# Optimization experiments

Measured on AMD Instinct MI355X. Metric: run time of the kernel, lower is better.

Reference implementation:

```python
import jax, jax.numpy as jnp
import numpy as np

N_NODES = 20000   # max_childs
N_EDGES = 640000
FEAT = 256        # node_feat_size
HID = 128         # node_hidden_size
NUM_SEM = 57
EDGE_TYPES = 4
EDGE_FEAT = 8


def setup_inputs() -> dict:
    key = jax.random.key(0)
    ks = jax.random.split(key, 10)
    inp = {
        "child_feats": jax.random.normal(ks[0], (1, N_NODES, FEAT + NUM_SEM), jnp.float32),
        "child_exists": jnp.ones((1, N_NODES, 1), jnp.float32),
        "edge_type_onehot": jax.random.uniform(ks[1], (1, N_EDGES, EDGE_TYPES), jnp.float32),
        "edge_feats": jax.random.normal(ks[2], (1, N_EDGES, EDGE_FEAT), jnp.float32),
        "edge_indices": jax.random.randint(ks[3], (1, N_EDGES, 2), 0, N_NODES, jnp.int64 if jax.config.jax_enable_x64 else jnp.int32),
        "W_child": jax.random.normal(ks[4], (FEAT + NUM_SEM, HID), jnp.float32) * 0.05,
        "b_child": jnp.zeros((HID,), jnp.float32),
        "W_edge0": jax.random.normal(ks[5], (2 * HID + EDGE_FEAT + EDGE_TYPES, HID), jnp.float32) * 0.05,
        "b_edge0": jnp.zeros((HID,), jnp.float32),
        "W_edge1": jax.random.normal(ks[6], (2 * HID + EDGE_FEAT + EDGE_TYPES, HID), jnp.float32) * 0.05,
        "b_edge1": jnp.zeros((HID,), jnp.float32),
        "W_parent": jax.random.normal(ks[7], (3 * HID, FEAT), jnp.float32) * 0.05,
        "b_parent": jnp.zeros((FEAT,), jnp.float32),
    }
    return inp


def reference(child_feats, child_exists, edge_type_onehot, edge_feats, edge_indices,
              W_child, b_child, W_edge0, b_edge0, W_edge1, b_edge1, W_parent, b_parent):
    # child_op + existence mask: [1, N, FEAT+NUM_SEM] -> [N, HID]
    h = jax.nn.relu(child_feats @ W_child + b_child) * child_exists
    h = h[0]  # batch_size is hard-coded to 1 in the original module

    # symmetric_type == 'max': pool over children
    iter_parent_feats = [jnp.max(h, axis=0)]

    # edge features: cat(edge_type_onehot, edge_feats) -> [E, ET+EF]
    ef = jnp.concatenate([edge_type_onehot[0], edge_feats[0]], axis=1)
    src = edge_indices[0, :, 0]
    dst = edge_indices[0, :, 1]

    for W, b in ((W_edge0, b_edge0), (W_edge1, b_edge1)):
        # gather -> per-edge MLP: [E, 2*HID + ET + EF] -> [E, HID]
        msg = jax.nn.relu(jnp.concatenate([h[src], h[dst], ef], axis=1) @ W + b)
        # edge_symmetric_type == 'max' with zero-initialized out buffer:
        # result = max(0, segment_max(msg)) per node
        h = jnp.maximum(jax.ops.segment_max(msg, src, num_segments=N_NODES), 0.0)
        iter_parent_feats.append(jnp.max(h, axis=0))

    parent = jnp.concatenate(iter_parent_feats)[None, :]  # [1, 3*HID]
    return jax.nn.relu(parent @ W_parent + b_parent)       # [1, FEAT]
```

## Files before the change

### kernel.cpp

```cpp
#include <hip/hip_runtime.h>

#define N_NODES   20000
#define N_EDGES   640000
#define CF        313
#define KC        320
#define ROWB      640

typedef __attribute__((ext_vector_type(8))) short short8;
typedef __attribute__((ext_vector_type(4))) float f32x4;
typedef __attribute__((ext_vector_type(4))) unsigned short u16x4;
typedef _Float16 h2 __attribute__((ext_vector_type(2)));

static __device__ __forceinline__ unsigned short f2bf(float f) {
    unsigned u = __float_as_uint(f);
    u = u + 0x7FFFu + ((u >> 16) & 1u);
    return (unsigned short)(u >> 16);
}
static __device__ __forceinline__ int pkh(float a, float b) {
    h2 h; h.x = (_Float16)a; h.y = (_Float16)b;
    return __builtin_bit_cast(int, h);
}
static __device__ __forceinline__ h2 bch(int v) { return __builtin_bit_cast(h2, v); }
static __device__ __forceinline__ float dot2f(h2 a, h2 b, float c) {
    return __builtin_amdgcn_fdot2(a, b, c, false);
}

__global__ void setup_kernel(const float* __restrict__ Wc,
                             const float* __restrict__ We0,
                             const float* __restrict__ We1,
                             const int* __restrict__ eidx,
                             const float* __restrict__ cf,
                             unsigned short* __restrict__ WcT,
                             unsigned short* __restrict__ Wab0,
                             unsigned short* __restrict__ Wab1,
                             unsigned* __restrict__ hist,
                             unsigned short* __restrict__ cfp) {
    const int b = blockIdx.x, tid = threadIdx.x;
    if (b < 416) {
        int g = b * 256 + tid;
        if (g < 128 * KC) {
            int n = g / KC, k = g % KC;
            WcT[g] = f2bf(k < CF ? Wc[k * 128 + n] : 0.f);
        } else if (g < 128 * KC + 32768) {
            int h = g - 128 * KC;
            int n = h >> 7, k = h & 127;
            Wab0[h] = f2bf(n < 128 ? We0[k * 128 + n] : We0[(128 + k) * 128 + (n - 128)]);
        } else {
            int h = g - 128 * KC - 32768;
            int n = h >> 7, k = h & 127;
            Wab1[h] = f2bf(n < 128 ? We1[k * 128 + n] : We1[(128 + k) * 128 + (n - 128)]);
        }
    } else if (b < 2916) {
        int e = (b - 416) * 256 + tid;
        if (e < N_EDGES) atomicAdd(hist + eidx[2 * e], 1u);
    } else {
        int g = (b - 2916) * 256 + tid;
        if (g < 800000) {
            int node = g / 40, c = g - node * 40;
            const float* base = cf + (size_t)node * CF;
            short8 v = {};
            #pragma unroll
            for (int kk = 0; kk < 8; ++kk) {
                int k = c * 8 + kk;
                if (k < CF) v[kk] = (short)f2bf(base[k]);
            }
            *(short8*)(cfp + (size_t)g * 8) = v;
        }
    }
}

__global__ void scan_kernel(const unsigned* __restrict__ hist,
                            unsigned* __restrict__ cursor,
                            unsigned* __restrict__ cstart) {
    __shared__ unsigned part[1024];
    int t = threadIdx.x;
    unsigned loc[20];
    unsigned s = 0;
    int base = t * 20;
    if (t < 1000) {
        #pragma unroll
        for (int i = 0; i < 20; ++i) { loc[i] = hist[base + i]; s += loc[i]; }
    }
    part[t] = s;
    __syncthreads();
    for (int off = 1; off < 1024; off <<= 1) {
        unsigned u = (t >= off) ? part[t - off] : 0u;
        __syncthreads();
        part[t] += u;
        __syncthreads();
    }
    if (t < 1000) {
        unsigned run = part[t] - s;
        #pragma unroll
        for (int i = 0; i < 20; ++i) {
            cursor[base + i] = run;
            cstart[base + i] = run;
            run += loc[i];
        }
    }
}

__global__ void scatter_kernel(const int* __restrict__ eidx,
                               const float* __restrict__ onehot,
                               const float* __restrict__ efeat,
                               unsigned* __restrict__ cursor,
                               int4* __restrict__ es) {
    int e = blockIdx.x * 256 + threadIdx.x;
    if (e >= N_EDGES) return;
    int2 sd = ((const int2*)eidx)[e];
    unsigned pos = atomicAdd(cursor + sd.x, 1u);
    float4 oh = *(const float4*)(onehot + 4 * (size_t)e);
    float4 ea = *(const float4*)(efeat + 8 * (size_t)e);
    float4 eb = *(const float4*)(efeat + 8 * (size_t)e + 4);
    int4 w0, w1;
    w0.x = sd.y;
    w0.y = pkh(oh.x, oh.y); w0.z = pkh(oh.z, oh.w); w0.w = pkh(ea.x, ea.y);
    w1.x = pkh(ea.z, ea.w); w1.y = pkh(eb.x, eb.y); w1.z = pkh(eb.z, eb.w); w1.w = 0;
    es[2 * (size_t)pos]     = w0;
    es[2 * (size_t)pos + 1] = w1;
}

__global__ __launch_bounds__(256, 2)
void child_gemm(const unsigned short* __restrict__ cfp,
                const float* __restrict__ exists,
                const unsigned short* __restrict__ WT,
                const float* __restrict__ bias,
                unsigned short* __restrict__ hbf,
                unsigned int* __restrict__ pmax) {
    __shared__ __align__(16) unsigned char Alds[64 * ROWB];

    const int tid  = threadIdx.x;
    const int lane = tid & 63;
    const int wave = tid >> 6;
    const int n0   = wave * 32;
    const int row0 = blockIdx.x * 64;

    short8 bfrag[10][2];
    {
        int col  = n0 + (lane & 15);
        int krow = (lane >> 4) * 8;
        #pragma unroll
        for (int ks = 0; ks < 10; ++ks)
            #pragma unroll
            for (int nt = 0; nt < 2; ++nt)
                bfrag[ks][nt] = *(const short8*)(WT + (col + nt * 16) * KC + ks * 32 + krow);
    }
    float bv[2];
    bv[0] = bias[n0 + (lane & 15)];
    bv[1] = bias[n0 + 16 + (lane & 15)];

    {
        int r = tid >> 2, p = tid & 3;
        int node = row0 + r;
        bool valid = node < N_NODES;
        unsigned rbase = r * ROWB;
        unsigned sw = (r & 7) << 4;
        #pragma unroll
        for (int i = 0; i < 10; ++i) {
            int c = p + i * 4;
            short8 v = {};
            if (valid) v = *(const short8*)(cfp + (size_t)node * KC + c * 8);
            *(short8*)(Alds + ((rbase + c * 16) ^ sw)) = v;
        }
    }
    __syncthreads();

    f32x4 acc[4][2] = {};
    {
        int arow = lane & 15;
        unsigned kb = (lane >> 4) * 16;
        #pragma unroll
        for (int ks = 0; ks < 10; ++ks)
            #pragma unroll
            for (int mt = 0; mt < 4; ++mt) {
                int row = mt * 16 + arow;
                short8 a = *(const short8*)(Alds + (((unsigned)row * ROWB + ks * 64 + kb) ^ ((row & 7) << 4)));
                acc[mt][0] = __builtin_amdgcn_mfma_f32_16x16x32_bf16(a, bfrag[ks][0], acc[mt][0], 0, 0, 0);
                acc[mt][1] = __builtin_amdgcn_mfma_f32_16x16x32_bf16(a, bfrag[ks][1], acc[mt][1], 0, 0, 0);
            }
    }

    {
        int rb = (lane >> 4) * 4;
        #pragma unroll
        for (int nt = 0; nt < 2; ++nt) {
            int col = n0 + nt * 16 + (lane & 15);
            float m = 0.f;
            #pragma unroll
            for (int mt = 0; mt < 4; ++mt)
                #pragma unroll
                for (int j = 0; j < 4; ++j) {
                    int node = row0 + mt * 16 + rb + j;
                    float v = 0.f;
                    if (node < N_NODES) {
                        v = fmaxf(acc[mt][nt][j] + bv[nt], 0.f) * exists[node];
                        hbf[node * 128 + col] = f2bf(v);
                    }
                    m = fmaxf(m, v);
                }
            m = fmaxf(m, __shfl_xor(m, 16));
            m = fmaxf(m, __shfl_xor(m, 32));
            if ((lane >> 4) == 0)
                atomicMax(pmax + col, __float_as_uint(m));
        }
    }
}

__global__ __launch_bounds__(256)
void gemmAB(const unsigned short* __restrict__ hbf,
            const unsigned short* __restrict__ WT,
            const float* __restrict__ bias,
            float* __restrict__ Afl,
            unsigned short* __restrict__ Bbf) {
    const int tid  = threadIdx.x;
    const int lane = tid & 63;
    const int wave = tid >> 6;
    const int n0   = wave * 64;
    const int row0 = blockIdx.x * 64;
    const int krow = (lane >> 4) * 8;

    short8 bfrag[4][4];
    {
        int colb = n0 + (lane & 15);
        #pragma unroll
        for (int ks = 0; ks < 4; ++ks)
            #pragma unroll
            for (int nt = 0; nt < 4; ++nt)
                bfrag[ks][nt] = *(const short8*)(WT + (colb + nt * 16) * 128 + ks * 32 + krow);
    }

    f32x4 acc[4][4] = {};
    #pragma unroll
    for (int ks = 0; ks < 4; ++ks)
        #pragma unroll
        for (int mt = 0; mt < 4; ++mt) {
            int row = row0 + mt * 16 + (lane & 15);
            row = min(row, N_NODES - 1);
            short8 a = *(const short8*)(hbf + (size_t)row * 128 + ks * 32 + krow);
            #pragma unroll
            for (int nt = 0; nt < 4; ++nt)
                acc[mt][nt] = __builtin_amdgcn_mfma_f32_16x16x32_bf16(a, bfrag[ks][nt], acc[mt][nt], 0, 0, 0);
        }

    {
        int rb = (lane >> 4) * 4;
        #pragma unroll
        for (int nt = 0; nt < 4; ++nt) {
            int col = n0 + nt * 16 + (lane & 15);
            float badd = (col < 128) ? bias[col] : 0.f;
            #pragma unroll
            for (int mt = 0; mt < 4; ++mt)
                #pragma unroll
                for (int j = 0; j < 4; ++j) {
                    int row = row0 + mt * 16 + rb + j;
                    if (row < N_NODES) {
                        float v = acc[mt][nt][j] + badd;
                        if (col < 128) Afl[(size_t)row * 128 + col] = v;
                        else           Bbf[(size_t)row * 128 + col - 128] = f2bf(v);
                    }
                }
        }
    }
}

__global__ __launch_bounds__(256)
void edge_pass(const unsigned short* __restrict__ Bbf,
               const float* __restrict__ Afl,
               const int4* __restrict__ es,
               const float* __restrict__ Wef,
               const unsigned* __restrict__ cstart,
               const unsigned* __restrict__ hist,
               unsigned short* __restrict__ hbf,
               unsigned* __restrict__ pslice) {
    __shared__ unsigned cmax[128];
    const int tid = threadIdx.x;
    if (tid < 128) cmax[tid] = 0;
    __syncthreads();

    const int s  = blockIdx.x * 8 + (tid >> 5);
    const int c0 = (tid & 31) * 4;

    h2 wf[6][4];
    #pragma unroll
    for (int kp = 0; kp < 6; ++kp)
        #pragma unroll
        for (int j = 0; j < 4; ++j) {
            h2 w;
            w.x = (_Float16)Wef[(2 * kp) * 128 + c0 + j];
            w.y = (_Float16)Wef[(2 * kp + 1) * 128 + c0 + j];
            wf[kp][j] = w;
        }

    float m0 = -1e30f, m1 = -1e30f, m2 = -1e30f, m3 = -1e30f;
    const unsigned cnt = hist[s];
    if (cnt) {
        const int4* p = es + 2 * (size_t)cstart[s];
        const unsigned last = cnt - 1;
        unsigned j1 = min(1u, last), j2 = min(2u, last), j3 = min(3u, last);
        int4 ra0 = p[0],      rb0 = p[1];
        int4 ra1 = p[2 * j1], rb1 = p[2 * j1 + 1];
        int4 ra2 = p[2 * j2], rb2 = p[2 * j2 + 1];
        int4 ra3 = p[2 * j3], rb3 = p[2 * j3 + 1];
        u16x4 b0 = *(const u16x4*)(Bbf + (size_t)(unsigned)ra0.x * 128 + c0);
        u16x4 b1 = *(const u16x4*)(Bbf + (size_t)(unsigned)ra1.x * 128 + c0);
        u16x4 b2 = *(const u16x4*)(Bbf + (size_t)(unsigned)ra2.x * 128 + c0);
        #pragma unroll 4
        for (unsigned i = 0; i < cnt; ++i) {
            u16x4 b3 = *(const u16x4*)(Bbf + (size_t)(unsigned)ra3.x * 128 + c0);
            unsigned j4 = min(i + 4, last);
            int4 ra4 = p[2 * j4], rb4 = p[2 * j4 + 1];

            h2 e0 = bch(ra0.y), e1 = bch(ra0.z), e2 = bch(ra0.w);
            h2 e3 = bch(rb0.x), e4 = bch(rb0.y), e5 = bch(rb0.z);

            float x0 = __uint_as_float(((unsigned)(unsigned short)b0[0]) << 16);
            float x1 = __uint_as_float(((unsigned)(unsigned short)b0[1]) << 16);
            float x2 = __uint_as_float(((unsigned)(unsigned short)b0[2]) << 16);
            float x3 = __uint_as_float(((unsigned)(unsigned short)b0[3]) << 16);
            x0 = dot2f(e0, wf[0][0], x0); x1 = dot2f(e0, wf[0][1], x1);
            x2 = dot2f(e0, wf[0][2], x2); x3 = dot2f(e0, wf[0][3], x3);
            x0 = dot2f(e1, wf[1][0], x0); x1 = dot2f(e1, wf[1][1], x1);
            x2 = dot2f(e1, wf[1][2], x2); x3 = dot2f(e1, wf[1][3], x3);
            x0 = dot2f(e2, wf[2][0], x0); x1 = dot2f(e2, wf[2][1], x1);
            x2 = dot2f(e2, wf[2][2], x2); x3 = dot2f(e2, wf[2][3], x3);
            x0 = dot2f(e3, wf[3][0], x0); x1 = dot2f(e3, wf[3][1], x1);
            x2 = dot2f(e3, wf[3][2], x2); x3 = dot2f(e3, wf[3][3], x3);
            x0 = dot2f(e4, wf[4][0], x0); x1 = dot2f(e4, wf[4][1], x1);
            x2 = dot2f(e4, wf[4][2], x2); x3 = dot2f(e4, wf[4][3], x3);
            x0 = dot2f(e5, wf[5][0], x0); x1 = dot2f(e5, wf[5][1], x1);
            x2 = dot2f(e5, wf[5][2], x2); x3 = dot2f(e5, wf[5][3], x3);
            m0 = fmaxf(m0, x0); m1 = fmaxf(m1, x1);
            m2 = fmaxf(m2, x2); m3 = fmaxf(m3, x3);

            ra0 = ra1; rb0 = rb1; ra1 = ra2; rb1 = rb2;
            ra2 = ra3; rb2 = rb3; ra3 = ra4; rb3 = rb4;
            b0 = b1; b1 = b2; b2 = b3;
        }
    }

    float4 a = *(const float4*)(Afl + (size_t)s * 128 + c0);
    float h0 = fmaxf(a.x + m0, 0.f), h1 = fmaxf(a.y + m1, 0.f);
    float h2v = fmaxf(a.z + m2, 0.f), h3 = fmaxf(a.w + m3, 0.f);

    unsigned lo = (unsigned)f2bf(h0) | ((unsigned)f2bf(h1) << 16);
    unsigned hi = (unsigned)f2bf(h2v) | ((unsigned)f2bf(h3) << 16);
    *(uint2*)(hbf + (size_t)s * 128 + c0) = make_uint2(lo, hi);

    float g0 = fmaxf(h0, __shfl_xor(h0, 32));
    float g1 = fmaxf(h1, __shfl_xor(h1, 32));
    float g2 = fmaxf(h2v, __shfl_xor(h2v, 32));
    float g3 = fmaxf(h3, __shfl_xor(h3, 32));
    if ((tid & 63) < 32) {
        atomicMax(&cmax[c0],     __float_as_uint(g0));
        atomicMax(&cmax[c0 + 1], __float_as_uint(g1));
        atomicMax(&cmax[c0 + 2], __float_as_uint(g2));
        atomicMax(&cmax[c0 + 3], __float_as_uint(g3));
    }
    __syncthreads();
    if (tid < 128) atomicMax(pslice + tid, cmax[tid]);
}

__global__ void final_gemm(const float* __restrict__ parent,
                           const float* __restrict__ Wp,
                           const float* __restrict__ bp,
                           float* __restrict__ out) {
    __shared__ float p[384];
    __shared__ float red[1024];
    int t = threadIdx.x;
    if (t < 384) p[t] = parent[t];
    __syncthreads();
    int col = t & 255, kc = t >> 8;
    float s = 0.f;
    for (int k = kc * 96; k < kc * 96 + 96; ++k) s += p[k] * Wp[k * 256 + col];
    red[t] = s;
    __syncthreads();
    if (kc == 0)
        out[col] = fmaxf(red[col] + red[col + 256] + red[col + 512] + red[col + 768] + bp[col], 0.f);
}

extern "C" void kernel_launch(void* const* d_in, const int* in_sizes, int n_in,
                              void* d_out, int out_size, void* d_ws, size_t ws_size,
                              hipStream_t stream) {
    const float* child_feats  = (const float*)d_in[0];
    const float* child_exists = (const float*)d_in[1];
    const float* onehot       = (const float*)d_in[2];
    const float* efeat        = (const float*)d_in[3];
    const int*   eidx         = (const int*)d_in[4];
    const float* Wc  = (const float*)d_in[5];
    const float* bc  = (const float*)d_in[6];
    const float* We0 = (const float*)d_in[7];
    const float* be0 = (const float*)d_in[8];
    const float* We1 = (const float*)d_in[9];
    const float* be1 = (const float*)d_in[10];
    const float* Wp  = (const float*)d_in[11];
    const float* bp  = (const float*)d_in[12];

    char* ws = (char*)d_ws;
    unsigned short* hbf    = (unsigned short*)(ws);
    float*          Afl    = (float*)(ws + 5120000);
    unsigned short* Bbf    = (unsigned short*)(ws + 15360000);
    int4*           es     = (int4*)(ws + 20480000);
    unsigned short* cfp    = (unsigned short*)(ws + 40960000);
    unsigned short* WcT    = (unsigned short*)(ws + 53760000);
    unsigned short* Wab0   = (unsigned short*)(ws + 53841920);
    unsigned short* Wab1   = (unsigned short*)(ws + 53907456);
    unsigned*       parent = (unsigned*)(ws + 53972992);
    unsigned*       hist   = (unsigned*)(ws + 53974528);
    unsigned*       cstart = (unsigned*)(ws + 54054528);
    unsigned*       cursor = (unsigned*)(ws + 54134528);

    const float* Wef0 = We0 + 256 * 128;
    const float* Wef1 = We1 + 256 * 128;

    hipMemsetAsync(parent, 0, 384 * 4, stream);
    hipMemsetAsync(hist, 0, N_NODES * 4, stream);

    setup_kernel<<<6041, 256, 0, stream>>>(Wc, We0, We1, eidx, child_feats,
                                           WcT, Wab0, Wab1, hist, cfp);
    scan_kernel<<<1, 1024, 0, stream>>>(hist, cursor, cstart);
    child_gemm<<<313, 256, 0, stream>>>(cfp, child_exists, WcT, bc, hbf, parent);
    scatter_kernel<<<2500, 256, 0, stream>>>(eidx, onehot, efeat, cursor, es);

    gemmAB<<<313, 256, 0, stream>>>(hbf, Wab0, be0, Afl, Bbf);
    edge_pass<<<2500, 256, 0, stream>>>(Bbf, Afl, es, Wef0, cstart, hist, hbf, parent + 128);

    gemmAB<<<313, 256, 0, stream>>>(hbf, Wab1, be1, Afl, Bbf);
    edge_pass<<<2500, 256, 0, stream>>>(Bbf, Afl, es, Wef1, cstart, hist, hbf, parent + 256);

    final_gemm<<<1, 1024, 0, stream>>>((const float*)parent, Wp, bp, (float*)d_out);
}
```

Measured before the change: 295.4 us.

## Balance edge_pass work with fixed-size edge windows staged in LDS

Rewrites the edge aggregation so each block loads its 8 nodes' contiguous edge records into shared memory in 256-edge windows and assigns each 32-lane group a fixed 32-edge slice. Source ids are stored in the edge record so groups can detect segment changes and flush partial maxima via order-preserving encoded atomicMax into per-node LDS buffers. The aim is to remove imbalance from varying node degree and to improve coalescing of the edge-record loads. In exchange it adds block syncs, LDS atomics and double-buffered prefetch complexity.

After: 300.2 us. About the same (+1.6%).

```diff
diff --git a/kernel.cpp b/kernel.cpp
--- a/kernel.cpp
+++ b/kernel.cpp
@@ -5,6 +5,7 @@
 #define CF        313
 #define KC        320
 #define ROWB      640
+#define WIN       256
 
 typedef __attribute__((ext_vector_type(8))) short short8;
 typedef __attribute__((ext_vector_type(4))) float f32x4;
@@ -23,6 +24,13 @@
 static __device__ __forceinline__ h2 bch(int v) { return __builtin_bit_cast(h2, v); }
 static __device__ __forceinline__ float dot2f(h2 a, h2 b, float c) {
     return __builtin_amdgcn_fdot2(a, b, c, false);
+}
+static __device__ __forceinline__ unsigned encf(float f) {
+    unsigned u = __float_as_uint(f);
+    return ((int)u >= 0) ? (u ^ 0x80000000u) : ~u;
+}
+static __device__ __forceinline__ float decf(unsigned u) {
+    return (u & 0x80000000u) ? __uint_as_float(u ^ 0x80000000u) : __uint_as_float(~u);
 }
 
 __global__ void setup_kernel(const float* __restrict__ Wc,
@@ -98,6 +106,7 @@
             run += loc[i];
         }
     }
+    if (t == 0) cstart[N_NODES] = N_EDGES;
 }
 
 __global__ void scatter_kernel(const int* __restrict__ eidx,
@@ -115,7 +124,8 @@
     int4 w0, w1;
     w0.x = sd.y;
     w0.y = pkh(oh.x, oh.y); w0.z = pkh(oh.z, oh.w); w0.w = pkh(ea.x, ea.y);
-    w1.x = pkh(ea.z, ea.w); w1.y = pkh(eb.x, eb.y); w1.z = pkh(eb.z, eb.w); w1.w = 0;
+    w1.x = pkh(ea.z, ea.w); w1.y = pkh(eb.x, eb.y); w1.z = pkh(eb.z, eb.w);
+    w1.w = sd.x;
     es[2 * (size_t)pos]     = w0;
     es[2 * (size_t)pos + 1] = w1;
 }
@@ -269,16 +279,25 @@
                const int4* __restrict__ es,
                const float* __restrict__ Wef,
                const unsigned* __restrict__ cstart,
-               const unsigned* __restrict__ hist,
                unsigned short* __restrict__ hbf,
                unsigned* __restrict__ pslice) {
+    __shared__ int4 rec[WIN][2];
+    __shared__ unsigned cmax8[8 * 128];
     __shared__ unsigned cmax[128];
+
     const int tid = threadIdx.x;
+    const int g   = tid >> 5;
+    const int c0  = (tid & 31) * 4;
+    const int s0  = blockIdx.x * 8;
+    const unsigned NEGE = encf(-1e30f);
+
+    cmax8[tid] = NEGE; cmax8[tid + 256] = NEGE;
+    cmax8[tid + 512] = NEGE; cmax8[tid + 768] = NEGE;
     if (tid < 128) cmax[tid] = 0;
-    __syncthreads();
-
-    const int s  = blockIdx.x * 8 + (tid >> 5);
-    const int c0 = (tid & 31) * 4;
+
+    const unsigned base = cstart[s0];
+    const unsigned T    = cstart[s0 + 8] - base;
+    const int nw = (int)((T + (WIN - 1)) >> 8);
 
     h2 wf[6][4];
     #pragma unroll
@@ -291,27 +310,56 @@
             wf[kp][j] = w;
         }
 
-    float m0 = -1e30f, m1 = -1e30f, m2 = -1e30f, m3 = -1e30f;
-    const unsigned cnt = hist[s];
-    if (cnt) {
-        const int4* p = es + 2 * (size_t)cstart[s];
-        const unsigned last = cnt - 1;
-        unsigned j1 = min(1u, last), j2 = min(2u, last), j3 = min(3u, last);
-        int4 ra0 = p[0],      rb0 = p[1];
-        int4 ra1 = p[2 * j1], rb1 = p[2 * j1 + 1];
-        int4 ra2 = p[2 * j2], rb2 = p[2 * j2 + 1];
-        int4 ra3 = p[2 * j3], rb3 = p[2 * j3 + 1];
-        u16x4 b0 = *(const u16x4*)(Bbf + (size_t)(unsigned)ra0.x * 128 + c0);
-        u16x4 b1 = *(const u16x4*)(Bbf + (size_t)(unsigned)ra1.x * 128 + c0);
-        u16x4 b2 = *(const u16x4*)(Bbf + (size_t)(unsigned)ra2.x * 128 + c0);
-        #pragma unroll 4
-        for (unsigned i = 0; i < cnt; ++i) {
-            u16x4 b3 = *(const u16x4*)(Bbf + (size_t)(unsigned)ra3.x * 128 + c0);
-            unsigned j4 = min(i + 4, last);
-            int4 ra4 = p[2 * j4], rb4 = p[2 * j4 + 1];
-
-            h2 e0 = bch(ra0.y), e1 = bch(ra0.z), e2 = bch(ra0.w);
-            h2 e3 = bch(rb0.x), e4 = bch(rb0.y), e5 = bch(rb0.z);
+    {
+        int4 sa = {0, 0, 0, 0}, sb = {0, 0, 0, -1};
+        if ((unsigned)tid < T) {
+            const int4* q = es + 2 * (size_t)(base + (unsigned)tid);
+            sa = q[0]; sb = q[1];
+        }
+        rec[tid][0] = sa; rec[tid][1] = sb;
+    }
+    __syncthreads();
+
+    int cur = -1;
+    float m0 = 0.f, m1 = 0.f, m2 = 0.f, m3 = 0.f;
+    const int slot0 = g * 32;
+
+    for (int w = 0; w < nw; ++w) {
+        const bool more = (w + 1 < nw);
+        int4 sa = {0, 0, 0, 0}, sb = {0, 0, 0, -1};
+        if (more) {
+            unsigned j = (unsigned)((w + 1) * WIN + tid);
+            if (j < T) {
+                const int4* q = es + 2 * (size_t)(base + j);
+                sa = q[0]; sb = q[1];
+            }
+        }
+
+        int dE;
+        u16x4 b0, b1, b2, b3;
+        {
+            int dA = rec[slot0 + 0][0].x;
+            int dB = rec[slot0 + 1][0].x;
+            int dC = rec[slot0 + 2][0].x;
+            int dD = rec[slot0 + 3][0].x;
+            dE     = rec[slot0 + 4][0].x;
+            b0 = *(const u16x4*)(Bbf + (size_t)(unsigned)dA * 128 + c0);
+            b1 = *(const u16x4*)(Bbf + (size_t)(unsigned)dB * 128 + c0);
+            b2 = *(const u16x4*)(Bbf + (size_t)(unsigned)dC * 128 + c0);
+            b3 = *(const u16x4*)(Bbf + (size_t)(unsigned)dD * 128 + c0);
+        }
+        #pragma unroll
+        for (int i = 0; i < 32; ++i) {
+            int dn = 0;
+            if (i < 27) dn = rec[slot0 + i + 5][0].x;
+            u16x4 bn = b0;
+            if (i < 28) bn = *(const u16x4*)(Bbf + (size_t)(unsigned)dE * 128 + c0);
+
+            int4 ra  = rec[slot0 + i][0];
+            int4 rb_ = rec[slot0 + i][1];
+            h2 e0 = bch(ra.y),  e1 = bch(ra.z),  e2 = bch(ra.w);
+            h2 e3 = bch(rb_.x), e4 = bch(rb_.y), e5 = bch(rb_.z);
+            int srcid = rb_.w;
 
             float x0 = __uint_as_float(((unsigned)(unsigned short)b0[0]) << 16);
             float x1 = __uint_as_float(((unsigned)(unsigned short)b0[1]) << 16);
@@ -329,32 +377,58 @@
             x2 = dot2f(e4, wf[4][2], x2); x3 = dot2f(e4, wf[4][3], x3);
             x0 = dot2f(e5, wf[5][0], x0); x1 = dot2f(e5, wf[5][1], x1);
             x2 = dot2f(e5, wf[5][2], x2); x3 = dot2f(e5, wf[5][3], x3);
-            m0 = fmaxf(m0, x0); m1 = fmaxf(m1, x1);
-            m2 = fmaxf(m2, x2); m3 = fmaxf(m3, x3);
-
-            ra0 = ra1; rb0 = rb1; ra1 = ra2; rb1 = rb2;
-            ra2 = ra3; rb2 = rb3; ra3 = ra4; rb3 = rb4;
-            b0 = b1; b1 = b2; b2 = b3;
-        }
-    }
-
-    float4 a = *(const float4*)(Afl + (size_t)s * 128 + c0);
-    float h0 = fmaxf(a.x + m0, 0.f), h1 = fmaxf(a.y + m1, 0.f);
-    float h2v = fmaxf(a.z + m2, 0.f), h3 = fmaxf(a.w + m3, 0.f);
-
-    unsigned lo = (unsigned)f2bf(h0) | ((unsigned)f2bf(h1) << 16);
-    unsigned hi = (unsigned)f2bf(h2v) | ((unsigned)f2bf(h3) << 16);
-    *(uint2*)(hbf + (size_t)s * 128 + c0) = make_uint2(lo, hi);
-
-    float g0 = fmaxf(h0, __shfl_xor(h0, 32));
-    float g1 = fmaxf(h1, __shfl_xor(h1, 32));
-    float g2 = fmaxf(h2v, __shfl_xor(h2v, 32));
-    float g3 = fmaxf(h3, __shfl_xor(h3, 32));
-    if ((tid & 63) < 32) {
-        atomicMax(&cmax[c0],     __float_as_uint(g0));
-        atomicMax(&cmax[c0 + 1], __float_as_uint(g1));
-        atomicMax(&cmax[c0 + 2], __float_as_uint(g2));
-        atomicMax(&cmax[c0 + 3], __float_as_uint(g3));
+
+            if (srcid != cur) {
+                if (cur >= 0) {
+                    unsigned* p8 = cmax8 + ((unsigned)(cur - s0) << 7) + c0;
+                    atomicMax(p8,     encf(m0));
+                    atomicMax(p8 + 1, encf(m1));
+                    atomicMax(p8 + 2, encf(m2));
+                    atomicMax(p8 + 3, encf(m3));
+                }
+                cur = srcid;
+                m0 = x0; m1 = x1; m2 = x2; m3 = x3;
+            } else {
+                m0 = fmaxf(m0, x0); m1 = fmaxf(m1, x1);
+                m2 = fmaxf(m2, x2); m3 = fmaxf(m3, x3);
+            }
+
+            b0 = b1; b1 = b2; b2 = b3; b3 = bn; dE = dn;
+        }
+
+        if (more) {
+            __syncthreads();
+            rec[tid][0] = sa; rec[tid][1] = sb;
+            __syncthreads();
+        }
+    }
+
+    if (cur >= 0) {
+        unsigned* p8 = cmax8 + ((unsigned)(cur - s0) << 7) + c0;
+        atomicMax(p8,     encf(m0));
+        atomicMax(p8 + 1, encf(m1));
+        atomicMax(p8 + 2, encf(m2));
+        atomicMax(p8 + 3, encf(m3));
+    }
+    __syncthreads();
+
+    {
+        const int s = s0 + g;
+        float4 a = *(const float4*)(Afl + (size_t)s * 128 + c0);
+        const unsigned* p8 = cmax8 + ((unsigned)g << 7) + c0;
+        float h0v = fmaxf(a.x + decf(p8[0]), 0.f);
+        float h1v = fmaxf(a.y + decf(p8[1]), 0.f);
+        float h2v = fmaxf(a.z + decf(p8[2]), 0.f);
+        float h3v = fmaxf(a.w + decf(p8[3]), 0.f);
+
+        unsigned lo = (unsigned)f2bf(h0v) | ((unsigned)f2bf(h1v) << 16);
+        unsigned hi = (unsigned)f2bf(h2v) | ((unsigned)f2bf(h3v) << 16);
+        *(uint2*)(hbf + (size_t)s * 128 + c0) = make_uint2(lo, hi);
+
+        atomicMax(&cmax[c0],     __float_as_uint(h0v));
+        atomicMax(&cmax[c0 + 1], __float_as_uint(h1v));
+        atomicMax(&cmax[c0 + 2], __float_as_uint(h2v));
+        atomicMax(&cmax[c0 + 3], __float_as_uint(h3v));
     }
     __syncthreads();
     if (tid < 128) atomicMax(pslice + tid, cmax[tid]);
@@ -407,7 +481,7 @@
     unsigned*       parent = (unsigned*)(ws + 53972992);
     unsigned*       hist   = (unsigned*)(ws + 53974528);
     unsigned*       cstart = (unsigned*)(ws + 54054528);
-    unsigned*       cursor = (unsigned*)(ws + 54134528);
+    unsigned*       cursor = (unsigned*)(ws + 54134592);
 
     const float* Wef0 = We0 + 256 * 128;
     const float* Wef1 = We1 + 256 * 128;
@@ -422,10 +496,10 @@
     scatter_kernel<<<2500, 256, 0, stream>>>(eidx, onehot, efeat, cursor, es);
 
     gemmAB<<<313, 256, 0, stream>>>(hbf, Wab0, be0, Afl, Bbf);
-    edge_pass<<<2500, 256, 0, stream>>>(Bbf, Afl, es, Wef0, cstart, hist, hbf, parent + 128);
+    edge_pass<<<2500, 256, 0, stream>>>(Bbf, Afl, es, Wef0, cstart, hbf, parent + 128);
 
     gemmAB<<<313, 256, 0, stream>>>(hbf, Wab1, be1, Afl, Bbf);
-    edge_pass<<<2500, 256, 0, stream>>>(Bbf, Afl, es, Wef1, cstart, hist, hbf, parent + 256);
+    edge_pass<<<2500, 256, 0, stream>>>(Bbf, Afl, es, Wef1, cstart, hbf, parent + 256);
 
     final_gemm<<<1, 1024, 0, stream>>>((const float*)parent, Wp, bp, (float*)d_out);
 }
```

## Deepen edge-pass prefetch pipeline and fold parent memset into scan

Applied to the files above, without the earlier changes.

Rewrites the edge_pass inner loop as a 12-way unrolled software pipeline with separate prefetch distances: destination indices twelve edges ahead, Bbf rows six ahead, and edge records three ahead. It also hoists the Afl load and asks for three blocks per CU through launch bounds. The parent memset moves into scan_kernel, and the child-feature packing drops its per-element bounds check for full chunks. These changes aim to hide gather latency and remove one memset launch, at the cost of more registers and possible spills under the tighter occupancy bound.

Result: faster. 278.3 us (-5.8%).

```diff
diff --git a/kernel.cpp b/kernel.cpp
--- a/kernel.cpp
+++ b/kernel.cpp
@@ -57,12 +57,13 @@
         int g = (b - 2916) * 256 + tid;
         if (g < 800000) {
             int node = g / 40, c = g - node * 40;
-            const float* base = cf + (size_t)node * CF;
+            const float* base = cf + (size_t)node * CF + c * 8;
             short8 v = {};
-            #pragma unroll
-            for (int kk = 0; kk < 8; ++kk) {
-                int k = c * 8 + kk;
-                if (k < CF) v[kk] = (short)f2bf(base[k]);
+            if (c < 39) {
+                #pragma unroll
+                for (int kk = 0; kk < 8; ++kk) v[kk] = (short)f2bf(base[kk]);
+            } else {
+                v[0] = (short)f2bf(base[0]);
             }
             *(short8*)(cfp + (size_t)g * 8) = v;
         }
@@ -71,9 +72,11 @@
 
 __global__ void scan_kernel(const unsigned* __restrict__ hist,
                             unsigned* __restrict__ cursor,
-                            unsigned* __restrict__ cstart) {
+                            unsigned* __restrict__ cstart,
+                            unsigned* __restrict__ parent) {
     __shared__ unsigned part[1024];
     int t = threadIdx.x;
+    if (t < 384) parent[t] = 0;
     unsigned loc[20];
     unsigned s = 0;
     int base = t * 20;
@@ -115,7 +118,8 @@
     int4 w0, w1;
     w0.x = sd.y;
     w0.y = pkh(oh.x, oh.y); w0.z = pkh(oh.z, oh.w); w0.w = pkh(ea.x, ea.y);
-    w1.x = pkh(ea.z, ea.w); w1.y = pkh(eb.x, eb.y); w1.z = pkh(eb.z, eb.w); w1.w = 0;
+    w1.x = pkh(ea.z, ea.w); w1.y = pkh(eb.x, eb.y); w1.z = pkh(eb.z, eb.w);
+    w1.w = 0;
     es[2 * (size_t)pos]     = w0;
     es[2 * (size_t)pos + 1] = w1;
 }
@@ -263,7 +267,7 @@
     }
 }
 
-__global__ __launch_bounds__(256)
+__global__ __launch_bounds__(256, 3)
 void edge_pass(const unsigned short* __restrict__ Bbf,
                const float* __restrict__ Afl,
                const int4* __restrict__ es,
@@ -280,6 +284,8 @@
     const int s  = blockIdx.x * 8 + (tid >> 5);
     const int c0 = (tid & 31) * 4;
 
+    float4 a = *(const float4*)(Afl + (size_t)s * 128 + c0);
+
     h2 wf[6][4];
     #pragma unroll
     for (int kp = 0; kp < 6; ++kp)
@@ -294,51 +300,66 @@
     float m0 = -1e30f, m1 = -1e30f, m2 = -1e30f, m3 = -1e30f;
     const unsigned cnt = hist[s];
     if (cnt) {
-        const int4* p = es + 2 * (size_t)cstart[s];
         const unsigned last = cnt - 1;
-        unsigned j1 = min(1u, last), j2 = min(2u, last), j3 = min(3u, last);
-        int4 ra0 = p[0],      rb0 = p[1];
-        int4 ra1 = p[2 * j1], rb1 = p[2 * j1 + 1];
-        int4 ra2 = p[2 * j2], rb2 = p[2 * j2 + 1];
-        int4 ra3 = p[2 * j3], rb3 = p[2 * j3 + 1];
-        u16x4 b0 = *(const u16x4*)(Bbf + (size_t)(unsigned)ra0.x * 128 + c0);
-        u16x4 b1 = *(const u16x4*)(Bbf + (size_t)(unsigned)ra1.x * 128 + c0);
-        u16x4 b2 = *(const u16x4*)(Bbf + (size_t)(unsigned)ra2.x * 128 + c0);
-        #pragma unroll 4
-        for (unsigned i = 0; i < cnt; ++i) {
-            u16x4 b3 = *(const u16x4*)(Bbf + (size_t)(unsigned)ra3.x * 128 + c0);
-            unsigned j4 = min(i + 4, last);
-            int4 ra4 = p[2 * j4], rb4 = p[2 * j4 + 1];
-
-            h2 e0 = bch(ra0.y), e1 = bch(ra0.z), e2 = bch(ra0.w);
-            h2 e3 = bch(rb0.x), e4 = bch(rb0.y), e5 = bch(rb0.z);
-
-            float x0 = __uint_as_float(((unsigned)(unsigned short)b0[0]) << 16);
-            float x1 = __uint_as_float(((unsigned)(unsigned short)b0[1]) << 16);
-            float x2 = __uint_as_float(((unsigned)(unsigned short)b0[2]) << 16);
-            float x3 = __uint_as_float(((unsigned)(unsigned short)b0[3]) << 16);
-            x0 = dot2f(e0, wf[0][0], x0); x1 = dot2f(e0, wf[0][1], x1);
-            x2 = dot2f(e0, wf[0][2], x2); x3 = dot2f(e0, wf[0][3], x3);
-            x0 = dot2f(e1, wf[1][0], x0); x1 = dot2f(e1, wf[1][1], x1);
-            x2 = dot2f(e1, wf[1][2], x2); x3 = dot2f(e1, wf[1][3], x3);
-            x0 = dot2f(e2, wf[2][0], x0); x1 = dot2f(e2, wf[2][1], x1);
-            x2 = dot2f(e2, wf[2][2], x2); x3 = dot2f(e2, wf[2][3], x3);
-            x0 = dot2f(e3, wf[3][0], x0); x1 = dot2f(e3, wf[3][1], x1);
-            x2 = dot2f(e3, wf[3][2], x2); x3 = dot2f(e3, wf[3][3], x3);
-            x0 = dot2f(e4, wf[4][0], x0); x1 = dot2f(e4, wf[4][1], x1);
-            x2 = dot2f(e4, wf[4][2], x2); x3 = dot2f(e4, wf[4][3], x3);
-            x0 = dot2f(e5, wf[5][0], x0); x1 = dot2f(e5, wf[5][1], x1);
-            x2 = dot2f(e5, wf[5][2], x2); x3 = dot2f(e5, wf[5][3], x3);
-            m0 = fmaxf(m0, x0); m1 = fmaxf(m1, x1);
-            m2 = fmaxf(m2, x2); m3 = fmaxf(m3, x3);
-
-            ra0 = ra1; rb0 = rb1; ra1 = ra2; rb1 = rb2;
-            ra2 = ra3; rb2 = rb3; ra3 = ra4; rb3 = rb4;
-            b0 = b1; b1 = b2; b2 = b3;
-        }
-    }
-
-    float4 a = *(const float4*)(Afl + (size_t)s * 128 + c0);
+        const unsigned cb = cstart[s] * 32u;
+        const char* esb = (const char*)es;
+        const unsigned short* bbase = Bbf + c0;
+
+        unsigned dstv[12];
+        int4 ra[3], rb[3];
+        u16x4 bv[6];
+
+        #pragma unroll
+        for (int k = 0; k < 12; ++k)
+            dstv[k] = *(const unsigned*)(esb + cb + min((unsigned)k, last) * 32u);
+        #pragma unroll
+        for (int k = 0; k < 3; ++k) {
+            const int4* q = (const int4*)(esb + cb + min((unsigned)k, last) * 32u);
+            ra[k] = q[0]; rb[k] = q[1];
+        }
+        #pragma unroll
+        for (int k = 0; k < 6; ++k)
+            bv[k] = *(const u16x4*)(bbase + (size_t)dstv[k] * 128);
+
+        const unsigned niter = (cnt + 11) / 12;
+        for (unsigned it = 0; it < niter; ++it) {
+            const unsigned jb = it * 12;
+            #pragma unroll
+            for (int u = 0; u < 12; ++u) {
+                int4 RA = ra[u % 3], RB = rb[u % 3];
+                u16x4 B = bv[u % 6];
+                h2 e0 = bch(RA.y), e1 = bch(RA.z), e2 = bch(RA.w);
+                h2 e3 = bch(RB.x), e4 = bch(RB.y), e5 = bch(RB.z);
+
+                float x0 = __uint_as_float(((unsigned)(unsigned short)B[0]) << 16);
+                float x1 = __uint_as_float(((unsigned)(unsigned short)B[1]) << 16);
+                float x2 = __uint_as_float(((unsigned)(unsigned short)B[2]) << 16);
+                float x3 = __uint_as_float(((unsigned)(unsigned short)B[3]) << 16);
+                x0 = dot2f(e0, wf[0][0], x0); x1 = dot2f(e0, wf[0][1], x1);
+                x2 = dot2f(e0, wf[0][2], x2); x3 = dot2f(e0, wf[0][3], x3);
+                x0 = dot2f(e1, wf[1][0], x0); x1 = dot2f(e1, wf[1][1], x1);
+                x2 = dot2f(e1, wf[1][2], x2); x3 = dot2f(e1, wf[1][3], x3);
+                x0 = dot2f(e2, wf[2][0], x0); x1 = dot2f(e2, wf[2][1], x1);
+                x2 = dot2f(e2, wf[2][2], x2); x3 = dot2f(e2, wf[2][3], x3);
+                x0 = dot2f(e3, wf[3][0], x0); x1 = dot2f(e3, wf[3][1], x1);
+                x2 = dot2f(e3, wf[3][2], x2); x3 = dot2f(e3, wf[3][3], x3);
+                x0 = dot2f(e4, wf[4][0], x0); x1 = dot2f(e4, wf[4][1], x1);
+                x2 = dot2f(e4, wf[4][2], x2); x3 = dot2f(e4, wf[4][3], x3);
+                x0 = dot2f(e5, wf[5][0], x0); x1 = dot2f(e5, wf[5][1], x1);
+                x2 = dot2f(e5, wf[5][2], x2); x3 = dot2f(e5, wf[5][3], x3);
+                m0 = fmaxf(m0, x0); m1 = fmaxf(m1, x1);
+                m2 = fmaxf(m2, x2); m3 = fmaxf(m3, x3);
+
+                unsigned jd = min(jb + u + 12u, last);
+                dstv[u] = *(const unsigned*)(esb + cb + jd * 32u);
+                unsigned jr = min(jb + u + 3u, last);
+                const int4* q = (const int4*)(esb + cb + jr * 32u);
+                ra[u % 3] = q[0]; rb[u % 3] = q[1];
+                bv[u % 6] = *(const u16x4*)(bbase + (size_t)dstv[(u + 6) % 12] * 128);
+            }
+        }
+    }
+
     float h0 = fmaxf(a.x + m0, 0.f), h1 = fmaxf(a.y + m1, 0.f);
     float h2v = fmaxf(a.z + m2, 0.f), h3 = fmaxf(a.w + m3, 0.f);
 
@@ -407,17 +428,16 @@
     unsigned*       parent = (unsigned*)(ws + 53972992);
     unsigned*       hist   = (unsigned*)(ws + 53974528);
     unsigned*       cstart = (unsigned*)(ws + 54054528);
-    unsigned*       cursor = (unsigned*)(ws + 54134528);
+    unsigned*       cursor = (unsigned*)(ws + 54134592);
 
     const float* Wef0 = We0 + 256 * 128;
     const float* Wef1 = We1 + 256 * 128;
 
-    hipMemsetAsync(parent, 0, 384 * 4, stream);
     hipMemsetAsync(hist, 0, N_NODES * 4, stream);
 
     setup_kernel<<<6041, 256, 0, stream>>>(Wc, We0, We1, eidx, child_feats,
                                            WcT, Wab0, Wab1, hist, cfp);
-    scan_kernel<<<1, 1024, 0, stream>>>(hist, cursor, cstart);
+    scan_kernel<<<1, 1024, 0, stream>>>(hist, cursor, cstart, parent);
     child_gemm<<<313, 256, 0, stream>>>(cfp, child_exists, WcT, bc, hbf, parent);
     scatter_kernel<<<2500, 256, 0, stream>>>(eidx, onehot, efeat, cursor, es);
 
```
